# Performance work log

Measured on AMD Instinct MI355X. Metric: run time of the kernel, lower is better.

The kernel has to match this reference:

```python
import jax, jax.numpy as jnp
import numpy as np
from jax import lax

EPS = 1e-5


def _bn_eval(x, gamma, beta, mean, var, axis=1):
    # eval-mode batchnorm over channel axis
    shape = [1] * x.ndim
    shape[axis] = -1
    g = gamma.reshape(shape); b = beta.reshape(shape)
    m = mean.reshape(shape); v = var.reshape(shape)
    return (x - m) * (g * lax.rsqrt(v + EPS)) + b


def setup_inputs() -> dict:
    key = jax.random.key(0)
    ks = jax.random.split(key, 12)
    B, C, H, W, K = 16, 256, 128, 128, 5
    x_feat = jax.random.normal(ks[0], (B, C, H, W), jnp.float32)
    raw_img = jax.random.uniform(ks[1], (B, 3, H, W), jnp.float32)
    # img_feature: Conv2d(3,64,3,pad=1) + BN(64)
    w_conv1 = jax.random.normal(ks[2], (64, 3, 3, 3), jnp.float32) * 0.1
    b_conv1 = jax.random.normal(ks[3], (64,), jnp.float32) * 0.1
    g1 = jnp.ones((64,), jnp.float32)
    beta1 = jnp.zeros((64,), jnp.float32)
    m1 = jax.random.normal(ks[4], (64,), jnp.float32) * 0.1
    v1 = jax.random.uniform(ks[5], (64,), jnp.float32) + 0.5
    # conv_filter: Conv2d(64, C*K*K, 1) + BN(C*K*K)
    CK2 = C * K * K
    w_filt = jax.random.normal(ks[6], (CK2, 64), jnp.float32) * 0.05
    b_filt = jax.random.normal(ks[7], (CK2,), jnp.float32) * 0.05
    g2 = jnp.ones((CK2,), jnp.float32)
    beta2 = jnp.zeros((CK2,), jnp.float32)
    m2 = jax.random.normal(ks[8], (CK2,), jnp.float32) * 0.1
    v2 = jax.random.uniform(ks[9], (CK2,), jnp.float32) + 0.5
    return {"x_feat": x_feat, "raw_img": raw_img,
            "w_conv1": w_conv1, "b_conv1": b_conv1, "g1": g1, "beta1": beta1, "m1": m1, "v1": v1,
            "w_filt": w_filt, "b_filt": b_filt, "g2": g2, "beta2": beta2, "m2": m2, "v2": v2}


def reference(x_feat, raw_img, w_conv1, b_conv1, g1, beta1, m1, v1,
              w_filt, b_filt, g2, beta2, m2, v2):
    B, C, H, W = x_feat.shape
    K = int(round(np.sqrt(w_filt.shape[0] // C)))  # kernel_size
    pad = K // 2

    # ---- filter generation branch ----
    # Conv2d(3,64,3,pad=1)
    y = lax.conv_general_dilated(raw_img, w_conv1, (1, 1), ((1, 1), (1, 1)),
                                 dimension_numbers=("NCHW", "OIHW", "NCHW"))
    y = y + b_conv1[None, :, None, None]
    y = jax.nn.relu(_bn_eval(y, g1, beta1, m1, v1))
    img_feat = jnp.mean(y, axis=(2, 3))                        # (B, 64) global avg pool

    # 1x1 conv == dense: (B, C*K*K)
    df = img_feat @ w_filt.T + b_filt
    df = _bn_eval(df[:, :, None, None], g2, beta2, m2, v2)[:, :, 0, 0]
    df = df.reshape(B, C, K * K)
    # NOTE: original applies Softmax(dim=1) -> over the CHANNEL axis
    df = jax.nn.softmax(df, axis=1)                            # (B, C, K*K)

    # ---- per-sample dynamic depthwise conv ----
    x_pad = jnp.pad(x_feat, ((0, 0), (0, 0), (pad, pad), (pad, pad)), mode="reflect")
    filt = df.reshape(B, C, K, K)

    def dw(x, w):  # x: (C, Hp, Wp), w: (C, K, K)
        return lax.conv_general_dilated(
            x[None], w[:, None], (1, 1), "VALID",
            dimension_numbers=("NCHW", "OIHW", "NCHW"),
            feature_group_count=C)[0]

    out = jax.vmap(dw)(x_pad, filt)                            # (B, C, H, W)
    return out
```

## Files before the change

### kernel.cpp

```cpp
#include <hip/hip_runtime.h>

#define EPSV 1e-5f

typedef float f4 __attribute__((ext_vector_type(4)));
typedef float f2 __attribute__((ext_vector_type(2)));

#define B   16
#define CIN 3
#define C1  64
#define C   256
#define H   128
#define W   128
#define K   5
#define KK  25
#define FSTR 28

#define R1   8
#define WS1  32
#define TW1  36

__global__ __launch_bounds__(128) void k1_conv_pool(
    const float* __restrict__ raw, const float* __restrict__ wconv,
    const float* __restrict__ bconv, const float* __restrict__ g1,
    const float* __restrict__ be1, const float* __restrict__ m1,
    const float* __restrict__ v1, float* __restrict__ partial)
{
  const int bid   = blockIdx.x;
  const int b     = bid >> 6;
  const int chunk = (bid >> 2) & 15;
  const int wh    = bid & 3;
  const int tid   = threadIdx.x;

  __shared__ __align__(16) float t[CIN][R1 + 2][TW1];
  const float* rawb = raw + (size_t)b * CIN * H * W;
  for (int i = tid; i < CIN * (R1 + 2) * 34; i += 128) {
    int ic  = i / ((R1 + 2) * 34);
    int rem = i - ic * (R1 + 2) * 34;
    int r   = rem / 34;
    int cc  = rem - r * 34;
    int gr  = chunk * R1 + r - 1;
    int gc  = wh * WS1 + cc - 1;
    float val = 0.f;
    if ((unsigned)gr < H && (unsigned)gc < W)
      val = rawb[ic * H * W + gr * W + gc];
    t[ic][r][cc] = val;
  }
  __syncthreads();

  const int rp  = tid >> 5;
  const int grp = tid & 31;
  float wt[2][27], A[2], Bc[2];
#pragma unroll
  for (int g = 0; g < 2; ++g) {
    int c = grp * 2 + g;
#pragma unroll
    for (int k = 0; k < 27; ++k) wt[g][k] = wconv[c * 27 + k];
    float sc = g1[c] * rsqrtf(v1[c] + EPSV);
    A[g]  = sc;
    Bc[g] = (bconv[c] - m1[c]) * sc + be1[c];
  }

  f4 cur[CIN][4], nxt[CIN][4];
#pragma unroll
  for (int ic = 0; ic < CIN; ++ic)
#pragma unroll
    for (int r = 0; r < 4; ++r) cur[ic][r] = *(const f4*)&t[ic][2 * rp + r][0];

  float acc0 = 0.f, acc1 = 0.f;
#pragma unroll
  for (int j = 0; j < 8; ++j) {
#pragma unroll
    for (int ic = 0; ic < CIN; ++ic)
#pragma unroll
      for (int r = 0; r < 4; ++r) nxt[ic][r] = *(const f4*)&t[ic][2 * rp + r][4 * j + 4];

    float v[2][2][4];
#pragma unroll
    for (int q = 0; q < 2; ++q)
#pragma unroll
      for (int g = 0; g < 2; ++g)
#pragma unroll
        for (int p = 0; p < 4; ++p) v[q][g][p] = 0.f;

#pragma unroll
    for (int ic = 0; ic < CIN; ++ic) {
#pragma unroll
      for (int q = 0; q < 2; ++q) {
#pragma unroll
        for (int kh = 0; kh < 3; ++kh) {
          f4 a  = cur[ic][q + kh];
          f4 bb = nxt[ic][q + kh];
#pragma unroll
          for (int p = 0; p < 4; ++p) {
#pragma unroll
            for (int kw = 0; kw < 3; ++kw) {
              float e = (p + kw < 4) ? a[p + kw] : bb[p + kw - 4];
              v[q][0][p] += e * wt[0][ic * 9 + kh * 3 + kw];
              v[q][1][p] += e * wt[1][ic * 9 + kh * 3 + kw];
            }
          }
        }
      }
    }
#pragma unroll
    for (int q = 0; q < 2; ++q)
#pragma unroll
      for (int p = 0; p < 4; ++p) {
        acc0 += fmaxf(v[q][0][p] * A[0] + Bc[0], 0.f);
        acc1 += fmaxf(v[q][1][p] * A[1] + Bc[1], 0.f);
      }
#pragma unroll
    for (int ic = 0; ic < CIN; ++ic)
#pragma unroll
      for (int r = 0; r < 4; ++r) cur[ic][r] = nxt[ic][r];
  }

  __shared__ float red[4][C1];
  red[rp][grp * 2]     = acc0;
  red[rp][grp * 2 + 1] = acc1;
  __syncthreads();
  if (tid < C1) {
    float s = red[0][tid] + red[1][tid] + red[2][tid] + red[3][tid];
    partial[((size_t)((b * 16 + chunk) * 4 + wh)) * C1 + tid] = s;
  }
}

#define NCH 64

__global__ __launch_bounds__(256) void k2_filter(
    const float* __restrict__ partial, const float* __restrict__ wf,
    const float* __restrict__ bf, const float* __restrict__ g2,
    const float* __restrict__ be2, const float* __restrict__ m2,
    const float* __restrict__ v2, float* __restrict__ filt)
{
  const int b  = blockIdx.x / KK;
  const int kk = blockIdx.x - b * KK;
  const int c  = threadIdx.x;

  __shared__ float feat[C1];
  if (c < C1) {
    float s = 0.f;
#pragma unroll
    for (int ch = 0; ch < NCH; ++ch)
      s += partial[((size_t)b * NCH + ch) * C1 + c];
    feat[c] = s * (1.f / (H * W));
  }
  __syncthreads();

  const int idx = c * KK + kk;
  float v = bf[idx];
  const float* wr = wf + (size_t)idx * C1;
#pragma unroll
  for (int j = 0; j < C1; ++j) v += feat[j] * wr[j];
  v = (v - m2[idx]) * (g2[idx] * rsqrtf(v2[idx] + EPSV)) + be2[idx];

  __shared__ float red[256];
  red[c] = v;
  __syncthreads();
#pragma unroll
  for (int s = 128; s > 0; s >>= 1) {
    if (c < s) red[c] = fmaxf(red[c], red[c + s]);
    __syncthreads();
  }
  float mx = red[0];
  __syncthreads();
  float e = expf(v - mx);
  red[c] = e;
  __syncthreads();
#pragma unroll
  for (int s = 128; s > 0; s >>= 1) {
    if (c < s) red[c] += red[c + s];
    __syncthreads();
  }
  filt[((size_t)b * C + c) * FSTR + kk] = e / red[0];
}

#define R3  32
#define TW3 136
#define TH3 (R3 + 4)

__global__ __launch_bounds__(256, 8) void k3_dwconv(
    const float* __restrict__ x, const float* __restrict__ filt,
    float* __restrict__ out)
{
  const int bid = blockIdx.x;
  const int swz = (bid & 7) * 2048 + (bid >> 3);
  const int plane = swz >> 2;
  const int tile  = swz & 3;
  const int r0    = tile * R3;
  const int tid   = threadIdx.x;

  const float* xp = x   + (size_t)plane * H * W;
  float*       op = out + (size_t)plane * H * W;
  const float* fp = filt + (size_t)plane * FSTR;

  f4 fv[7];
#pragma unroll
  for (int i = 0; i < 7; ++i) fv[i] = *(const f4*)&fp[i << 2];

  __shared__ __align__(16) float t[TH3][TW3];

#pragma unroll
  for (int k = 0; k < 5; ++k) {
    int idx = tid + (k << 8);
    if (k < 4 || idx < TH3 * 32) {
      int r = idx >> 5, g = idx & 31;
      int gr = r0 + r - 2;
      gr = gr < 0 ? -gr : (gr >= H ? 2 * H - 2 - gr : gr);
      f4 v = *(const f4*)&xp[gr * W + (g << 2)];
      f2 lo = {v[0], v[1]};
      f2 hi = {v[2], v[3]};
      *(f2*)&t[r][(g << 2) + 2] = lo;
      *(f2*)&t[r][(g << 2) + 4] = hi;
    }
  }
  if (tid < TH3 * 4) {
    int r = tid >> 2, c = tid & 3;
    int cc = (c == 0) ? 0 : (c == 1) ? 1 : (c == 2) ? 130 : 131;
    int gc = (c == 0) ? 2 : (c == 1) ? 1 : (c == 2) ? 126 : 125;
    int gr = r0 + r - 2;
    gr = gr < 0 ? -gr : (gr >= H ? 2 * H - 2 - gr : gr);
    t[r][cc] = xp[gr * W + gc];
  }
  __syncthreads();

  const int w  = (tid & 31) << 2;
  const int rb = (tid >> 5) << 2;
  f4 acc[4];
#pragma unroll
  for (int q = 0; q < 4; ++q) acc[q] = (f4){0.f, 0.f, 0.f, 0.f};

#pragma unroll
  for (int tr = 0; tr < 8; ++tr) {
    f4 a  = *(const f4*)&t[rb + tr][w];
    f4 bb = *(const f4*)&t[rb + tr][w + 4];
#pragma unroll
    for (int q = 0; q < 4; ++q) {
      if (tr - q < 0 || tr - q > 4) continue;
      const int ki = tr - q;
#pragma unroll
      for (int p = 0; p < 4; ++p) {
#pragma unroll
        for (int j = 0; j < 5; ++j) {
          float e = (p + j < 4) ? a[p + j] : bb[p + j - 4];
          const int k = ki * 5 + j;
          acc[q][p] += e * fv[k >> 2][k & 3];
        }
      }
    }
  }
#pragma unroll
  for (int q = 0; q < 4; ++q)
    __builtin_nontemporal_store(acc[q], (f4*)&op[(r0 + rb + q) * W + w]);
}

extern "C" void kernel_launch(void* const* d_in, const int* in_sizes, int n_in,
                              void* d_out, int out_size, void* d_ws, size_t ws_size,
                              hipStream_t stream) {
  const float* x_feat = (const float*)d_in[0];
  const float* raw    = (const float*)d_in[1];
  const float* wconv  = (const float*)d_in[2];
  const float* bconv  = (const float*)d_in[3];
  const float* g1     = (const float*)d_in[4];
  const float* be1    = (const float*)d_in[5];
  const float* m1     = (const float*)d_in[6];
  const float* v1     = (const float*)d_in[7];
  const float* wf     = (const float*)d_in[8];
  const float* bf     = (const float*)d_in[9];
  const float* g2     = (const float*)d_in[10];
  const float* be2    = (const float*)d_in[11];
  const float* m2     = (const float*)d_in[12];
  const float* v2     = (const float*)d_in[13];
  float* out = (float*)d_out;

  float* partial = (float*)d_ws;
  float* filt    = partial + B * NCH * C1;

  k1_conv_pool<<<B * 16 * 4, 128, 0, stream>>>(raw, wconv, bconv, g1, be1, m1, v1, partial);
  k2_filter  <<<B * KK, 256, 0, stream>>>(partial, wf, bf, g2, be2, m2, v2, filt);
  k3_dwconv  <<<B * C * (H / R3), 256, 0, stream>>>(x_feat, filt, out);
}
```

Measured before the change: 127.0 us.

## Add weight-prep kernel, coalesce filter weights, use direct global-to-LDS loads in depthwise conv

A new prep kernel transposes the 1x1 filter weights and the 3x3 conv weights and precomputes the BN scale and shift, so later kernels read those weights with coalesced accesses. The depthwise conv stages rows into an unpadded LDS tile with global_load_lds. Reflect padding moves into register shuffles at tile edges, with the edge lane remapping which columns it stores. Occupancy hint drops from 8 to 6. This adds one extra launch, and the reflect remapping carries correctness risk.

```diff
diff --git a/kernel.cpp b/kernel.cpp
--- a/kernel.cpp
+++ b/kernel.cpp
@@ -15,15 +15,49 @@
 #define KK  25
 #define FSTR 28
 
+__global__ __launch_bounds__(256) void k0_prep(
+    const float* __restrict__ wconv, const float* __restrict__ bconv,
+    const float* __restrict__ g1, const float* __restrict__ be1,
+    const float* __restrict__ m1, const float* __restrict__ v1,
+    const float* __restrict__ wf,
+    float* __restrict__ wconvT, float* __restrict__ Ag,
+    float* __restrict__ Bg, float* __restrict__ wfT)
+{
+  const int bid = blockIdx.x, tid = threadIdx.x;
+  if (bid < 100) {
+    const int kk = bid >> 2;
+    const int c0 = (bid & 3) << 6;
+    __shared__ float tl[64][65];
+    for (int i = tid; i < 64 * 64; i += 256) {
+      int cl = i >> 6, j = i & 63;
+      tl[cl][j] = wf[((size_t)(c0 + cl) * KK + kk) * C1 + j];
+    }
+    __syncthreads();
+    for (int i = tid; i < 64 * 64; i += 256) {
+      int j = i >> 6, cl = i & 63;
+      wfT[(size_t)j * (C * KK) + kk * C + c0 + cl] = tl[cl][j];
+    }
+  } else {
+    for (int i = tid; i < 27 * 64; i += 256) {
+      int k = i >> 6, c = i & 63;
+      wconvT[k * 64 + c] = wconv[c * 27 + k];
+    }
+    if (tid < C1) {
+      float sc = g1[tid] * rsqrtf(v1[tid] + EPSV);
+      Ag[tid] = sc;
+      Bg[tid] = (bconv[tid] - m1[tid]) * sc + be1[tid];
+    }
+  }
+}
+
 #define R1   8
 #define WS1  32
 #define TW1  36
 
 __global__ __launch_bounds__(128) void k1_conv_pool(
-    const float* __restrict__ raw, const float* __restrict__ wconv,
-    const float* __restrict__ bconv, const float* __restrict__ g1,
-    const float* __restrict__ be1, const float* __restrict__ m1,
-    const float* __restrict__ v1, float* __restrict__ partial)
+    const float* __restrict__ raw, const float* __restrict__ wconvT,
+    const float* __restrict__ Ag, const float* __restrict__ Bg,
+    float* __restrict__ partial)
 {
   const int bid   = blockIdx.x;
   const int b     = bid >> 6;
@@ -51,13 +85,14 @@
   const int grp = tid & 31;
   float wt[2][27], A[2], Bc[2];
 #pragma unroll
+  for (int k = 0; k < 27; ++k) {
+    wt[0][k] = wconvT[k * 64 + grp * 2];
+    wt[1][k] = wconvT[k * 64 + grp * 2 + 1];
+  }
+#pragma unroll
   for (int g = 0; g < 2; ++g) {
-    int c = grp * 2 + g;
-#pragma unroll
-    for (int k = 0; k < 27; ++k) wt[g][k] = wconv[c * 27 + k];
-    float sc = g1[c] * rsqrtf(v1[c] + EPSV);
-    A[g]  = sc;
-    Bc[g] = (bconv[c] - m1[c]) * sc + be1[c];
+    A[g]  = Ag[grp * 2 + g];
+    Bc[g] = Bg[grp * 2 + g];
   }
 
   f4 cur[CIN][4], nxt[CIN][4];
@@ -128,7 +163,7 @@
 #define NCH 64
 
 __global__ __launch_bounds__(256) void k2_filter(
-    const float* __restrict__ partial, const float* __restrict__ wf,
+    const float* __restrict__ partial, const float* __restrict__ wfT,
     const float* __restrict__ bf, const float* __restrict__ g2,
     const float* __restrict__ be2, const float* __restrict__ m2,
     const float* __restrict__ v2, float* __restrict__ filt)
@@ -149,9 +184,9 @@
 
   const int idx = c * KK + kk;
   float v = bf[idx];
-  const float* wr = wf + (size_t)idx * C1;
-#pragma unroll
-  for (int j = 0; j < C1; ++j) v += feat[j] * wr[j];
+#pragma unroll
+  for (int j = 0; j < C1; ++j)
+    v += feat[j] * wfT[(size_t)j * (C * KK) + kk * C + c];
   v = (v - m2[idx]) * (g2[idx] * rsqrtf(v2[idx] + EPSV)) + be2[idx];
 
   __shared__ float red[256];
@@ -176,10 +211,9 @@
 }
 
 #define R3  32
-#define TW3 136
-#define TH3 (R3 + 4)
-
-__global__ __launch_bounds__(256, 8) void k3_dwconv(
+#define TH3 36
+
+__global__ __launch_bounds__(256, 6) void k3_dwconv(
     const float* __restrict__ x, const float* __restrict__ filt,
     float* __restrict__ out)
 {
@@ -189,6 +223,8 @@
   const int tile  = swz & 3;
   const int r0    = tile * R3;
   const int tid   = threadIdx.x;
+  const int lane  = tid & 63;
+  const int wv    = tid >> 6;
 
   const float* xp = x   + (size_t)plane * H * W;
   float*       op = out + (size_t)plane * H * W;
@@ -198,34 +234,28 @@
 #pragma unroll
   for (int i = 0; i < 7; ++i) fv[i] = *(const f4*)&fp[i << 2];
 
-  __shared__ __align__(16) float t[TH3][TW3];
-
-#pragma unroll
-  for (int k = 0; k < 5; ++k) {
-    int idx = tid + (k << 8);
-    if (k < 4 || idx < TH3 * 32) {
-      int r = idx >> 5, g = idx & 31;
-      int gr = r0 + r - 2;
-      gr = gr < 0 ? -gr : (gr >= H ? 2 * H - 2 - gr : gr);
-      f4 v = *(const f4*)&xp[gr * W + (g << 2)];
-      f2 lo = {v[0], v[1]};
-      f2 hi = {v[2], v[3]};
-      *(f2*)&t[r][(g << 2) + 2] = lo;
-      *(f2*)&t[r][(g << 2) + 4] = hi;
-    }
-  }
-  if (tid < TH3 * 4) {
-    int r = tid >> 2, c = tid & 3;
-    int cc = (c == 0) ? 0 : (c == 1) ? 1 : (c == 2) ? 130 : 131;
-    int gc = (c == 0) ? 2 : (c == 1) ? 1 : (c == 2) ? 126 : 125;
+  __shared__ __align__(16) float t[TH3][W];
+
+  for (int i = wv; i < TH3 / 2; i += 4) {
+    int r  = 2 * i + (lane >> 5);
     int gr = r0 + r - 2;
     gr = gr < 0 ? -gr : (gr >= H ? 2 * H - 2 - gr : gr);
-    t[r][cc] = xp[gr * W + gc];
-  }
-  __syncthreads();
-
-  const int w  = (tid & 31) << 2;
-  const int rb = (tid >> 5) << 2;
+    const float* gsrc = xp + gr * W + ((lane & 31) << 2);
+    __builtin_amdgcn_global_load_lds(
+        (const __attribute__((address_space(1))) void*)gsrc,
+        (__attribute__((address_space(3))) void*)&t[2 * i][0],
+        16, 0, 0);
+  }
+  __syncthreads();
+
+  const int g    = tid & 31;
+  const int w    = g << 2;
+  const bool edge = (g == 31);
+  const int bcol = edge ? 0   : w + 4;
+  const int colA = edge ? 126 : w + 2;
+  const int colB = edge ? 0   : w + 4;
+  const int rb   = (tid >> 5) << 2;
+
   f4 acc[4];
 #pragma unroll
   for (int q = 0; q < 4; ++q) acc[q] = (f4){0.f, 0.f, 0.f, 0.f};
@@ -233,25 +263,37 @@
 #pragma unroll
   for (int tr = 0; tr < 8; ++tr) {
     f4 a  = *(const f4*)&t[rb + tr][w];
-    f4 bb = *(const f4*)&t[rb + tr][w + 4];
+    f4 bb = *(const f4*)&t[rb + tr][bcol];
+    float wa[6], wb[6];
+    wa[0] = a[0]; wa[1] = a[1]; wa[2] = a[2]; wa[3] = a[3];
+    wa[4] = edge ? a[2]  : bb[0];
+    wa[5] = edge ? a[1]  : bb[1];
+    wb[0] = edge ? bb[2] : a[2];
+    wb[1] = edge ? bb[1] : a[3];
+    wb[2] = bb[0]; wb[3] = bb[1]; wb[4] = bb[2]; wb[5] = bb[3];
 #pragma unroll
     for (int q = 0; q < 4; ++q) {
       if (tr - q < 0 || tr - q > 4) continue;
       const int ki = tr - q;
 #pragma unroll
-      for (int p = 0; p < 4; ++p) {
-#pragma unroll
-        for (int j = 0; j < 5; ++j) {
-          float e = (p + j < 4) ? a[p + j] : bb[p + j - 4];
-          const int k = ki * 5 + j;
-          acc[q][p] += e * fv[k >> 2][k & 3];
-        }
+      for (int j = 0; j < 5; ++j) {
+        const int kq = ki * 5 + j;
+        const float fk = fv[kq >> 2][kq & 3];
+        acc[q][0] += wa[j]     * fk;
+        acc[q][1] += wa[j + 1] * fk;
+        acc[q][2] += wb[j]     * fk;
+        acc[q][3] += wb[j + 1] * fk;
       }
     }
   }
 #pragma unroll
-  for (int q = 0; q < 4; ++q)
-    __builtin_nontemporal_store(acc[q], (f4*)&op[(r0 + rb + q) * W + w]);
+  for (int q = 0; q < 4; ++q) {
+    const int row = r0 + rb + q;
+    f2 vA = {acc[q][0], acc[q][1]};
+    f2 vB = {acc[q][2], acc[q][3]};
+    __builtin_nontemporal_store(vA, (f2*)&op[row * W + colA]);
+    __builtin_nontemporal_store(vB, (f2*)&op[row * W + colB]);
+  }
 }
 
 extern "C" void kernel_launch(void* const* d_in, const int* in_sizes, int n_in,
@@ -275,8 +317,14 @@
 
   float* partial = (float*)d_ws;
   float* filt    = partial + B * NCH * C1;
-
-  k1_conv_pool<<<B * 16 * 4, 128, 0, stream>>>(raw, wconv, bconv, g1, be1, m1, v1, partial);
-  k2_filter  <<<B * KK, 256, 0, stream>>>(partial, wf, bf, g2, be2, m2, v2, filt);
+  float* wconvT  = filt + B * C * FSTR;
+  float* Ag      = wconvT + 27 * 64;
+  float* Bg      = Ag + 64;
+  float* wfT     = Bg + 64;
+
+  k0_prep    <<<101, 256, 0, stream>>>(wconv, bconv, g1, be1, m1, v1, wf,
+                                       wconvT, Ag, Bg, wfT);
+  k1_conv_pool<<<B * 16 * 4, 128, 0, stream>>>(raw, wconvT, Ag, Bg, partial);
+  k2_filter  <<<B * KK, 256, 0, stream>>>(partial, wfT, bf, g2, be2, m2, v2, filt);
   k3_dwconv  <<<B * C * (H / R3), 256, 0, stream>>>(x_feat, filt, out);
 }
```

Result: faster. 124.3 us (-2.1%).
